# Kernel tuning notes

Hardware: AMD Instinct MI355X
Metric: run time of the kernel (lower is better)

Reference implementation:

```python
import jax, jax.numpy as jnp
import numpy as np

N = 50000
E = 500000
IN_DIM = 384
HID = 256
HEADS = 4
OUT_DIM = 128
NEG_SLOPE = 0.2


def _glorot(key, shape):
    fan_in, fan_out = shape[0], shape[-1]
    lim = jnp.sqrt(6.0 / (fan_in + fan_out))
    return jax.random.uniform(key, shape, jnp.float32, -lim, lim)


def setup_inputs() -> dict:
    key = jax.random.key(0)
    ks = jax.random.split(key, 16)
    x = jax.random.normal(ks[0], (N, IN_DIM), jnp.float32)
    node_attr = jax.random.normal(ks[1], (N, 2), jnp.float32)
    edge_index = jax.random.randint(ks[2], (2, E), 0, N, jnp.int64)
    return {
        "x": x,
        "node_attr": node_attr,
        "edge_index": edge_index,
        # node_encoder: Linear(386 -> 384)
        "enc_W": _glorot(ks[3], (IN_DIM + 2, IN_DIM)),
        "enc_b": jnp.zeros((IN_DIM,), jnp.float32),
        # gat1: 384 -> 4 heads x 256, concat
        "W1": _glorot(ks[4], (IN_DIM, HEADS * HID)),
        "a_src1": _glorot(ks[5], (HEADS, HID)),
        "a_dst1": _glorot(ks[6], (HEADS, HID)),
        "b1": jnp.zeros((HEADS * HID,), jnp.float32),
        # gat2: 1024 -> 1 head x 128, mean (concat=False)
        "W2": _glorot(ks[7], (HEADS * HID, OUT_DIM)),
        "a_src2": _glorot(ks[8], (1, OUT_DIM)),
        "a_dst2": _glorot(ks[9], (1, OUT_DIM)),
        "b2": jnp.zeros((OUT_DIM,), jnp.float32),
    }


def gat_conv(x, src, dst, W, a_src, a_dst, bias, heads, out_ch, concat):
    # x: [N, F]; src/dst: [E'] (self-loops already included)
    n = x.shape[0]
    h = (x @ W).reshape(n, heads, out_ch)          # [N, H, C]
    alpha_s = jnp.einsum('nhc,hc->nh', h, a_src)   # [N, H]
    alpha_d = jnp.einsum('nhc,hc->nh', h, a_dst)
    e = alpha_s[src] + alpha_d[dst]                # [E', H]
    e = jnp.where(e >= 0, e, NEG_SLOPE * e)        # LeakyReLU(0.2)
    # segment softmax over incoming edges of each destination node
    m = jax.ops.segment_max(e, dst, num_segments=n)
    e = jnp.exp(e - m[dst])
    denom = jax.ops.segment_sum(e, dst, num_segments=n)
    alpha = e / (denom[dst] + 1e-16)               # [E', H]
    msg = h[src] * alpha[:, :, None]               # [E', H, C]
    out = jax.ops.segment_sum(msg, dst, num_segments=n)  # [N, H, C]
    out = out.reshape(n, heads * out_ch) if concat else out.mean(axis=1)
    return out + bias


def reference(x, node_attr, edge_index, enc_W, enc_b,
              W1, a_src1, a_dst1, b1, W2, a_src2, a_dst2, b2):
    n = x.shape[0]
    # node encoder on [x ; node_attr]
    h = jnp.concatenate([x, node_attr], axis=-1) @ enc_W + enc_b
    # add self-loops once (PyG GATConv default add_self_loops=True)
    loop = jnp.arange(n, dtype=edge_index.dtype)
    src = jnp.concatenate([edge_index[0], loop])
    dst = jnp.concatenate([edge_index[1], loop])
    h = gat_conv(h, src, dst, W1, a_src1, a_dst1, b1, HEADS, HID, True)
    h = jax.nn.elu(h)
    out = gat_conv(h, src, dst, W2, a_src2, a_dst2, b2, 1, OUT_DIM, False)
    return out
```

## Files before the change

### kernel.cpp

```cpp
#include <hip/hip_runtime.h>
#include <hip/hip_bf16.h>
#include <type_traits>


#define NN 50000
#define NE 500000
#define EP (NE + NN)

typedef __hip_bfloat16 bf16;
typedef short short8 __attribute__((ext_vector_type(8)));
typedef __bf16 bf16x8 __attribute__((ext_vector_type(8)));
typedef float f32x4 __attribute__((ext_vector_type(4)));

__device__ __forceinline__ float b2f(bf16 v) { return __bfloat162float(v); }
__device__ __forceinline__ bf16  f2b(float v) { return __float2bfloat16(v); }
__device__ __forceinline__ unsigned short f2bu(float v) {
  bf16 b = __float2bfloat16(v);
  return *reinterpret_cast<unsigned short*>(&b);
}

__device__ __forceinline__ float ldf(const void* p, size_t i, bool f32) {
  return f32 ? ((const float*)p)[i] : b2f(((const bf16*)p)[i]);
}

__device__ __forceinline__ float bflo(unsigned u) { return __uint_as_float(u << 16); }
__device__ __forceinline__ float bfhi(unsigned u) { return __uint_as_float(u & 0xffff0000u); }

__device__ __forceinline__ float leaky(float v) { return v >= 0.f ? v : 0.2f * v; }

__device__ __forceinline__ void gload_lds16(const void* g, void* l) {
  __builtin_amdgcn_global_load_lds(
      (const __attribute__((address_space(1))) void*)g,
      (__attribute__((address_space(3))) void*)l, 16, 0, 0);
}

__global__ void k_detect(const unsigned int* __restrict__ ei,
                         const unsigned int* __restrict__ xw,
                         unsigned int* __restrict__ eflag,
                         unsigned int* __restrict__ fflag) {
  const int b = blockIdx.x;
  if (b < 512) {
    unsigned int acc = 0;
    for (int i = b * 256 + threadIdx.x; i < NE; i += 512 * 256)
      acc |= ei[2 * i + 1];
    if (acc) atomicOr(eflag, 1u);
  } else {
    unsigned int acc = 0;
    for (int i = (b - 512) * 256 + threadIdx.x; i < (1 << 20); i += 256 * 256) {
      unsigned int e = (xw[i] >> 7) & 0xFF;
      if (e > 0xA0) acc = 1;
    }
    if (acc) atomicOr(fflag, 1u);
  }
}

__global__ void k_convert(const int* __restrict__ ei, const unsigned int* __restrict__ flag,
                          int* __restrict__ esrc, int* __restrict__ edst,
                          int* __restrict__ deg) {
  int e = blockIdx.x * 256 + threadIdx.x;
  if (e >= EP) return;
  int s, d;
  if (e < NE) {
    if (*flag) { s = ei[e]; d = ei[NE + e]; }
    else { const long long* e64 = (const long long*)ei; s = (int)e64[e]; d = (int)e64[NE + e]; }
    s = min(max(s, 0), NN - 1);
    d = min(max(d, 0), NN - 1);
  } else {
    s = d = e - NE;
  }
  esrc[e] = s;
  edst[e] = d;
  atomicAdd(&deg[d], 1);
}

__global__ void k_pack_cat(const void* __restrict__ x, const void* __restrict__ na,
                           bf16* __restrict__ catp, const unsigned int* __restrict__ fflag) {
  const bool f32 = (*fflag != 0);
  const int total = NN * 104;
  for (int g = blockIdx.x * 256 + threadIdx.x; g < total; g += gridDim.x * 256) {
    int n = g / 104, r = g - n * 104;
    int c = r * 4;
    float v0 = 0.f, v1 = 0.f, v2 = 0.f, v3 = 0.f;
    if (c < 384) {
      if (f32) {
        const float4 f = *(const float4*)((const float*)x + (size_t)n * 384 + c);
        v0 = f.x; v1 = f.y; v2 = f.z; v3 = f.w;
      } else {
        const bf16* xb = (const bf16*)x + (size_t)n * 384 + c;
        v0 = b2f(xb[0]); v1 = b2f(xb[1]); v2 = b2f(xb[2]); v3 = b2f(xb[3]);
      }
    } else if (c == 384) {
      v0 = ldf(na, (size_t)n * 2 + 0, f32);
      v1 = ldf(na, (size_t)n * 2 + 1, f32);
    }
    ushort2 o0, o1;
    o0.x = f2bu(v0); o0.y = f2bu(v1);
    o1.x = f2bu(v2); o1.y = f2bu(v3);
    ushort2* dst = (ushort2*)((unsigned short*)catp + (size_t)n * 416 + c);
    dst[0] = o0; dst[1] = o1;
  }
}

__global__ void k_pack_w3(const void* __restrict__ Wenc, bf16* __restrict__ encWp,
                          const void* __restrict__ W1, bf16* __restrict__ W1p,
                          const void* __restrict__ W2, bf16* __restrict__ W2p,
                          const unsigned int* __restrict__ fflag) {
  const bool f32 = (*fflag != 0);
  const int s0 = 416 * 384, s1 = 384 * 1024, s2 = 1024 * 128;
  int g = blockIdx.x * 256 + threadIdx.x;
  const void* W; bf16* Wp; int K, N, i;
  if (g < s0)                { W = Wenc; Wp = encWp; K = 386;  N = 384;  i = g; }
  else if (g < s0 + s1)      { W = W1;   Wp = W1p;   K = 384;  N = 1024; i = g - s0; }
  else if (g < s0 + s1 + s2) { W = W2;   Wp = W2p;   K = 1024; N = 128;  i = g - s0 - s1; }
  else return;
  int kb = i / (N * 32);
  int rem = i - kb * N * 32;
  int n = rem >> 5, kk = rem & 31;
  int k = kb * 32 + kk;
  float v = (k < K) ? ldf(W, (size_t)k * N + n, f32) : 0.f;
  Wp[i] = f2b(v);
}

template<bool ADD_BIAS, bool ALPHA, int NH, typename CT>
__global__ __launch_bounds__(256) void gemm_mfma(
    const bf16* __restrict__ A, int lda,
    const bf16* __restrict__ Bp,
    const void* __restrict__ bias,
    const void* __restrict__ a_srcp, const void* __restrict__ a_dstp,
    float* __restrict__ as_out, float* __restrict__ ad_out,
    CT* __restrict__ C,
    int M, int N, int K,
    const unsigned int* __restrict__ fflag) {
  const bool xf32 = (ADD_BIAS || ALPHA) ? (*fflag != 0) : false;
  __shared__ short As[128 * 32];
  __shared__ short Bs[128 * 32];
  const int t = threadIdx.x;
  const int lane = t & 63, wave = t >> 6;
  const int wm = wave & 1, wn = wave >> 1;
  const int quad = lane >> 4, l15 = lane & 15;
  const int m0 = blockIdx.x * 128, n0 = blockIdx.y * 128;

  f32x4 acc[4][4];
#pragma unroll
  for (int i = 0; i < 4; ++i)
#pragma unroll
    for (int j = 0; j < 4; ++j) acc[i][j] = (f32x4){0.f, 0.f, 0.f, 0.f};

  const int c0 = t, c1 = t + 256;
  const int arow0 = min(m0 + (c0 >> 2), M - 1), akoff0 = (c0 & 3) * 8;
  const int arow1 = min(m0 + (c1 >> 2), M - 1), akoff1 = (c1 & 3) * 8;

  for (int k0 = 0; k0 < K; k0 += 32) {
    gload_lds16((const short*)A + (size_t)arow0 * lda + k0 + akoff0, &As[c0 * 8]);
    gload_lds16((const short*)A + (size_t)arow1 * lda + k0 + akoff1, &As[c1 * 8]);
    {
      const short* base = (const short*)Bp + ((size_t)(k0 >> 5) * N + n0) * 32;
      gload_lds16(base + c0 * 8, &Bs[c0 * 8]);
      gload_lds16(base + c1 * 8, &Bs[c1 * 8]);
    }
    __syncthreads();
    bf16x8 af[4], bfr[4];
#pragma unroll
    for (int mi = 0; mi < 4; ++mi)
      af[mi] = *reinterpret_cast<const bf16x8*>(&As[(wm * 64 + mi * 16 + l15) * 32 + quad * 8]);
#pragma unroll
    for (int ni = 0; ni < 4; ++ni)
      bfr[ni] = *reinterpret_cast<const bf16x8*>(&Bs[(wn * 64 + ni * 16 + l15) * 32 + quad * 8]);
#pragma unroll
    for (int mi = 0; mi < 4; ++mi)
#pragma unroll
      for (int ni = 0; ni < 4; ++ni)
        acc[mi][ni] = __builtin_amdgcn_mfma_f32_16x16x32_bf16(af[mi], bfr[ni], acc[mi][ni], 0, 0, 0);
    __syncthreads();
  }

#pragma unroll
  for (int mi = 0; mi < 4; ++mi) {
#pragma unroll
    for (int ni = 0; ni < 4; ++ni) {
      const int gn = n0 + wn * 64 + ni * 16 + l15;
      float bv = ADD_BIAS ? ldf(bias, gn, xf32) : 0.f;
#pragma unroll
      for (int r = 0; r < 4; ++r) {
        const int gm = m0 + wm * 64 + mi * 16 + quad * 4 + r;
        if (gm < M) {
          float v = acc[mi][ni][r] + bv;
          if constexpr (std::is_same<CT, float>::value)
            C[(size_t)gm * N + gn] = v;
          else
            C[(size_t)gm * N + gn] = f2b(v);
        }
      }
    }
  }

  if (ALPHA) {
    float avs[4], avd[4];
#pragma unroll
    for (int ni = 0; ni < 4; ++ni) {
      const int gn = n0 + wn * 64 + ni * 16 + l15;
      avs[ni] = ldf(a_srcp, gn, xf32);
      avd[ni] = ldf(a_dstp, gn, xf32);
    }
    const int head = (n0 + wn * 64) >> 8;
#pragma unroll
    for (int mi = 0; mi < 4; ++mi) {
#pragma unroll
      for (int r = 0; r < 4; ++r) {
        float ps = 0.f, pd = 0.f;
#pragma unroll
        for (int ni = 0; ni < 4; ++ni) {
          const float v = acc[mi][ni][r];
          ps = fmaf(v, avs[ni], ps);
          pd = fmaf(v, avd[ni], pd);
        }
#pragma unroll
        for (int off = 8; off > 0; off >>= 1) {
          ps += __shfl_down(ps, off, 16);
          pd += __shfl_down(pd, off, 16);
        }
        if (l15 == 0) {
          const int gm = m0 + wm * 64 + mi * 16 + quad * 4 + r;
          if (gm < M) {
            atomicAdd(&as_out[gm * NH + head], ps);
            atomicAdd(&ad_out[gm * NH + head], pd);
          }
        }
      }
    }
  }
}

#define SCAN_B 512
#define SCAN_NB ((NN + SCAN_B - 1) / SCAN_B)

__global__ __launch_bounds__(SCAN_B) void k_scan1(const int* __restrict__ deg,
                                                  int* __restrict__ row_ptr,
                                                  int* __restrict__ partial) {
  int b = blockIdx.x, t = threadIdx.x;
  int i = b * SCAN_B + t;
  int v = (i < NN) ? deg[i] : 0;
  int lane = t & 63, w = t >> 6;
  int x = v;
#pragma unroll
  for (int off = 1; off < 64; off <<= 1) {
    int y = __shfl_up(x, off, 64);
    if (lane >= off) x += y;
  }
  __shared__ int ws[8];
  if (lane == 63) ws[w] = x;
  __syncthreads();
  if (t == 0) {
    int run = 0;
#pragma unroll
    for (int j = 0; j < 8; ++j) { int tmp = ws[j]; ws[j] = run; run += tmp; }
    partial[b] = run;
  }
  __syncthreads();
  int excl = x - v + ws[w];
  if (i < NN) row_ptr[i] = excl;
}

__global__ void k_scan2(int* __restrict__ partial, int* __restrict__ row_ptr) {
  if (blockIdx.x == 0 && threadIdx.x == 0) {
    int run = 0;
    for (int j = 0; j < SCAN_NB; ++j) { int tmp = partial[j]; partial[j] = run; run += tmp; }
    row_ptr[NN] = run;
  }
}

__global__ __launch_bounds__(SCAN_B) void k_scan3(const int* __restrict__ partial,
                                                  int* __restrict__ row_ptr,
                                                  int* __restrict__ cursor) {
  int b = blockIdx.x, t = threadIdx.x;
  int i = b * SCAN_B + t;
  if (i < NN) {
    int v = row_ptr[i] + partial[b];
    row_ptr[i] = v;
    cursor[i] = v;
  }
}

__global__ void k_scatter(const int* __restrict__ esrc, const int* __restrict__ edst,
                          int* __restrict__ cursor, int* __restrict__ csr) {
  int e = blockIdx.x * 256 + threadIdx.x;
  if (e >= EP) return;
  int pos = atomicAdd(&cursor[edst[e]], 1);
  pos = min(max(pos, 0), EP - 1);
  csr[pos] = esrc[e];
}

__global__ __launch_bounds__(256) void k_agg1(
    const int* __restrict__ csr, const int* __restrict__ row_ptr,
    const float* __restrict__ as1, const float* __restrict__ ad1,
    const bf16* __restrict__ h1, const void* __restrict__ b1,
    bf16* __restrict__ act1, const unsigned int* __restrict__ fflag) {
  const bool f32 = (*fflag != 0);
  const int n = blockIdx.x, t = threadIdx.x;
  const int w = t >> 6, l = t & 63;
  const int start = row_ptr[n], end = row_ptr[n + 1];
  const float adn = ad1[n * 4 + w];
  const unsigned* hb = (const unsigned*)h1;
  const int coff = w * 128 + l * 2;

  float a0 = 0.f, a1 = 0.f, a2 = 0.f, a3 = 0.f, densum = 0.f;

  int idx = start;
  for (; idx + 4 <= end; idx += 4) {
    int s0 = csr[idx], s1 = csr[idx + 1], s2 = csr[idx + 2], s3 = csr[idx + 3];
    uint2 w0 = *(const uint2*)(hb + (size_t)s0 * 512 + coff);
    uint2 w1 = *(const uint2*)(hb + (size_t)s1 * 512 + coff);
    uint2 w2 = *(const uint2*)(hb + (size_t)s2 * 512 + coff);
    uint2 w3 = *(const uint2*)(hb + (size_t)s3 * 512 + coff);
    float p0 = __expf(leaky(as1[s0 * 4 + w] + adn));
    float p1 = __expf(leaky(as1[s1 * 4 + w] + adn));
    float p2 = __expf(leaky(as1[s2 * 4 + w] + adn));
    float p3 = __expf(leaky(as1[s3 * 4 + w] + adn));
    densum += (p0 + p1) + (p2 + p3);
    a0 = fmaf(bflo(w0.x), p0, a0); a1 = fmaf(bfhi(w0.x), p0, a1);
    a2 = fmaf(bflo(w0.y), p0, a2); a3 = fmaf(bfhi(w0.y), p0, a3);
    a0 = fmaf(bflo(w1.x), p1, a0); a1 = fmaf(bfhi(w1.x), p1, a1);
    a2 = fmaf(bflo(w1.y), p1, a2); a3 = fmaf(bfhi(w1.y), p1, a3);
    a0 = fmaf(bflo(w2.x), p2, a0); a1 = fmaf(bfhi(w2.x), p2, a1);
    a2 = fmaf(bflo(w2.y), p2, a2); a3 = fmaf(bfhi(w2.y), p2, a3);
    a0 = fmaf(bflo(w3.x), p3, a0); a1 = fmaf(bfhi(w3.x), p3, a1);
    a2 = fmaf(bflo(w3.y), p3, a2); a3 = fmaf(bfhi(w3.y), p3, a3);
  }
  for (; idx < end; ++idx) {
    int s0 = csr[idx];
    uint2 w0 = *(const uint2*)(hb + (size_t)s0 * 512 + coff);
    float p0 = __expf(leaky(as1[s0 * 4 + w] + adn));
    densum += p0;
    a0 = fmaf(bflo(w0.x), p0, a0); a1 = fmaf(bfhi(w0.x), p0, a1);
    a2 = fmaf(bflo(w0.y), p0, a2); a3 = fmaf(bfhi(w0.y), p0, a3);
  }

  const float inv = 1.f / (densum + 1e-16f);
  const int col = w * 256 + l * 4;
  float v0 = a0 * inv + ldf(b1, col + 0, f32);
  float v1 = a1 * inv + ldf(b1, col + 1, f32);
  float v2 = a2 * inv + ldf(b1, col + 2, f32);
  float v3 = a3 * inv + ldf(b1, col + 3, f32);
  v0 = v0 > 0.f ? v0 : expm1f(v0);
  v1 = v1 > 0.f ? v1 : expm1f(v1);
  v2 = v2 > 0.f ? v2 : expm1f(v2);
  v3 = v3 > 0.f ? v3 : expm1f(v3);
  unsigned lo = (unsigned)f2bu(v0) | ((unsigned)f2bu(v1) << 16);
  unsigned hi = (unsigned)f2bu(v2) | ((unsigned)f2bu(v3) << 16);
  unsigned long long ow = (unsigned long long)lo | ((unsigned long long)hi << 32);
  __builtin_nontemporal_store(
      ow, (unsigned long long*)((unsigned short*)act1 + (size_t)n * 1024 + col));
}

__global__ __launch_bounds__(256) void k_agg2(
    const int* __restrict__ csr, const int* __restrict__ row_ptr,
    const float* __restrict__ as2, const float* __restrict__ ad2,
    const bf16* __restrict__ h2, const void* __restrict__ b2v,
    float* __restrict__ out, const unsigned int* __restrict__ fflag) {
  const bool f32 = (*fflag != 0);
  const int t = threadIdx.x;
  const int wv = t >> 6, l = t & 63;
  const int n = blockIdx.x * 4 + wv;
  const int start = row_ptr[n], end = row_ptr[n + 1];
  const float adn = ad2[n];
  const unsigned* hb = (const unsigned*)h2;
  float a0 = 0.f, a1 = 0.f, densum = 0.f;

  int idx = start;
  for (; idx + 2 <= end; idx += 2) {
    const int s0 = __builtin_amdgcn_readfirstlane(csr[idx]);
    const int s1 = __builtin_amdgcn_readfirstlane(csr[idx + 1]);
    const unsigned w0 = hb[(size_t)s0 * 64 + l];
    const unsigned w1 = hb[(size_t)s1 * 64 + l];
    const float p0 = __expf(leaky(as2[s0] + adn));
    const float p1 = __expf(leaky(as2[s1] + adn));
    densum += p0 + p1;
    a0 = fmaf(bflo(w0), p0, a0); a1 = fmaf(bfhi(w0), p0, a1);
    a0 = fmaf(bflo(w1), p1, a0); a1 = fmaf(bfhi(w1), p1, a1);
  }
  if (idx < end) {
    const int s0 = __builtin_amdgcn_readfirstlane(csr[idx]);
    const unsigned w0 = hb[(size_t)s0 * 64 + l];
    const float p0 = __expf(leaky(as2[s0] + adn));
    densum += p0;
    a0 = fmaf(bflo(w0), p0, a0); a1 = fmaf(bfhi(w0), p0, a1);
  }

  const float inv = 1.f / (densum + 1e-16f);
  float2 o;
  o.x = a0 * inv + ldf(b2v, l * 2 + 0, f32);
  o.y = a1 * inv + ldf(b2v, l * 2 + 1, f32);
  unsigned long long u;
  __builtin_memcpy(&u, &o, 8);
  __builtin_nontemporal_store(u, (unsigned long long*)(out + (size_t)n * 128 + l * 2));
}

extern "C" void kernel_launch(void* const* d_in, const int* in_sizes, int n_in,
                              void* d_out, int out_size, void* d_ws, size_t ws_size,
                              hipStream_t stream) {
  const void* x       = d_in[0];
  const void* na      = d_in[1];
  const int*  ei      = (const int*)d_in[2];
  const void* enc_W   = d_in[3];
  const void* enc_b   = d_in[4];
  const void* W1      = d_in[5];
  const void* a_src1  = d_in[6];
  const void* a_dst1  = d_in[7];
  const void* b1      = d_in[8];
  const void* W2      = d_in[9];
  const void* a_src2  = d_in[10];
  const void* a_dst2  = d_in[11];
  const void* b2      = d_in[12];
  float* out = (float*)d_out;

  size_t off = 0;
  char* ws = (char*)d_ws;
  auto alloc = [&](size_t bytes) -> void* {
    void* p = ws + off;
    off += (bytes + 255) & ~(size_t)255;
    return p;
  };
  bf16*  h1      = (bf16*)alloc((size_t)NN * 1024 * 2);
  bf16*  act1    = (bf16*)alloc((size_t)NN * 1024 * 2);
  bf16*  catp    = act1;
  bf16*  h0      = (bf16*)alloc((size_t)NN * 384 * 2);
  bf16*  h2      = (bf16*)alloc((size_t)NN * 128 * 2);
  bf16*  encWp   = (bf16*)alloc((size_t)416 * 384 * 2);
  bf16*  W1p     = (bf16*)alloc((size_t)384 * 1024 * 2);
  bf16*  W2p     = (bf16*)alloc((size_t)1024 * 128 * 2);
  int*   esrc    = (int*)alloc((size_t)EP * 4);
  int*   edst    = (int*)alloc((size_t)EP * 4);
  int*   csr     = (int*)alloc((size_t)EP * 4);
  char*  zero_base = ws + off;
  unsigned int* eflag = (unsigned int*)alloc(4);
  unsigned int* fflag = (unsigned int*)alloc(4);
  int*   deg     = (int*)alloc((size_t)NN * 4);
  float* as1     = (float*)alloc((size_t)NN * 4 * 4);
  float* ad1     = (float*)alloc((size_t)NN * 4 * 4);
  float* as2     = (float*)alloc((size_t)NN * 4);
  float* ad2     = (float*)alloc((size_t)NN * 4);
  size_t zero_len = (size_t)((ws + off) - zero_base);
  int*   row_ptr = (int*)alloc((size_t)(NN + 1) * 4);
  int*   cursor  = (int*)alloc((size_t)NN * 4);
  int*   partial = (int*)alloc((size_t)SCAN_NB * 4);
  (void)ws_size; (void)in_sizes; (void)n_in; (void)out_size;

  (void)hipMemsetAsync(zero_base, 0, zero_len, stream);

  const int EB = (EP + 255) / 256;
  const int MB = (NN + 127) / 128;

  k_detect<<<768, 256, 0, stream>>>((const unsigned int*)ei, (const unsigned int*)x,
                                    eflag, fflag);

  k_convert<<<EB, 256, 0, stream>>>(ei, eflag, esrc, edst, deg);
  k_scan1<<<SCAN_NB, SCAN_B, 0, stream>>>(deg, row_ptr, partial);
  k_scan2<<<1, 64, 0, stream>>>(partial, row_ptr);
  k_scan3<<<SCAN_NB, SCAN_B, 0, stream>>>(partial, row_ptr, cursor);
  k_scatter<<<EB, 256, 0, stream>>>(esrc, edst, cursor, csr);

  k_pack_cat<<<8192, 256, 0, stream>>>(x, na, catp, fflag);
  k_pack_w3<<<2672, 256, 0, stream>>>(enc_W, encWp, W1, W1p, W2, W2p, fflag);

  gemm_mfma<true, false, 1, bf16><<<dim3(MB, 3), 256, 0, stream>>>(
      catp, 416, encWp, enc_b, nullptr, nullptr, nullptr, nullptr,
      h0, NN, 384, 416, fflag);
  gemm_mfma<false, true, 4, bf16><<<dim3(MB, 8), 256, 0, stream>>>(
      h0, 384, W1p, nullptr, a_src1, a_dst1, as1, ad1,
      h1, NN, 1024, 384, fflag);

  k_agg1<<<NN, 256, 0, stream>>>(csr, row_ptr, as1, ad1, h1, b1, act1, fflag);

  gemm_mfma<false, true, 1, bf16><<<dim3(MB, 1), 256, 0, stream>>>(
      act1, 1024, W2p, nullptr, a_src2, a_dst2, as2, ad2,
      h2, NN, 128, 1024, fflag);

  k_agg2<<<NN / 4, 256, 0, stream>>>(csr, row_ptr, as2, ad2, h2, b2, out, fflag);
}
```

Baseline: 653.5 us.

## Fuse preprocessing kernels into one cooperative kernel with grid syncs

Replaces eight small preprocessing launches (dtype detection, edge conversion, degree scan, CSR scatter, input and weight packing) with a single cooperative kernel that uses grid.sync between phases. It keeps the old multi-kernel path as a fallback if the cooperative launch fails. The aim is to remove per-launch overhead and idle gaps between tiny kernels. In exchange it adds grid-wide barrier costs and runs the work on a fixed 1024-block grid.

```diff
diff --git a/kernel.cpp b/kernel.cpp
--- a/kernel.cpp
+++ b/kernel.cpp
@@ -1,11 +1,14 @@
 #include <hip/hip_runtime.h>
 #include <hip/hip_bf16.h>
+#include <hip/hip_cooperative_groups.h>
 #include <type_traits>
 
 
 #define NN 50000
 #define NE 500000
 #define EP (NE + NN)
+
+namespace cg = cooperative_groups;
 
 typedef __hip_bfloat16 bf16;
 typedef short short8 __attribute__((ext_vector_type(8)));
@@ -32,6 +35,162 @@
   __builtin_amdgcn_global_load_lds(
       (const __attribute__((address_space(1))) void*)g,
       (__attribute__((address_space(3))) void*)l, 16, 0, 0);
+}
+
+__device__ __forceinline__ void convert_item(int e, bool ef, const int* ei,
+                                             int* esrc, int* edst, int* deg) {
+  int s, d;
+  if (e < NE) {
+    if (ef) { s = ei[e]; d = ei[NE + e]; }
+    else { const long long* e64 = (const long long*)ei; s = (int)e64[e]; d = (int)e64[NE + e]; }
+    s = min(max(s, 0), NN - 1);
+    d = min(max(d, 0), NN - 1);
+  } else {
+    s = d = e - NE;
+  }
+  esrc[e] = s;
+  edst[e] = d;
+  atomicAdd(&deg[d], 1);
+}
+
+__device__ __forceinline__ void pack_cat_item(int g, bool f32, const void* x,
+                                              const void* na, bf16* catp) {
+  int n = g / 104, r = g - n * 104;
+  int c = r * 4;
+  float v0 = 0.f, v1 = 0.f, v2 = 0.f, v3 = 0.f;
+  if (c < 384) {
+    if (f32) {
+      const float4 f = *(const float4*)((const float*)x + (size_t)n * 384 + c);
+      v0 = f.x; v1 = f.y; v2 = f.z; v3 = f.w;
+    } else {
+      const bf16* xb = (const bf16*)x + (size_t)n * 384 + c;
+      v0 = b2f(xb[0]); v1 = b2f(xb[1]); v2 = b2f(xb[2]); v3 = b2f(xb[3]);
+    }
+  } else if (c == 384) {
+    v0 = ldf(na, (size_t)n * 2 + 0, f32);
+    v1 = ldf(na, (size_t)n * 2 + 1, f32);
+  }
+  ushort2 o0, o1;
+  o0.x = f2bu(v0); o0.y = f2bu(v1);
+  o1.x = f2bu(v2); o1.y = f2bu(v3);
+  ushort2* dst = (ushort2*)((unsigned short*)catp + (size_t)n * 416 + c);
+  dst[0] = o0; dst[1] = o1;
+}
+
+#define PW_S0 (416 * 384)
+#define PW_S1 (384 * 1024)
+#define PW_S2 (1024 * 128)
+
+__device__ __forceinline__ void pack_w3_item(int i, bool f32,
+                                             const void* Wenc, bf16* encWp,
+                                             const void* W1, bf16* W1p,
+                                             const void* W2, bf16* W2p) {
+  const void* W; bf16* Wp; int K, N, ii;
+  if (i < PW_S0)               { W = Wenc; Wp = encWp; K = 386;  N = 384;  ii = i; }
+  else if (i < PW_S0 + PW_S1)  { W = W1;   Wp = W1p;   K = 384;  N = 1024; ii = i - PW_S0; }
+  else                         { W = W2;   Wp = W2p;   K = 1024; N = 128;  ii = i - PW_S0 - PW_S1; }
+  int kb = ii / (N * 32);
+  int rem = ii - kb * N * 32;
+  int n = rem >> 5, kk = rem & 31;
+  int k = kb * 32 + kk;
+  float v = (k < K) ? ldf(W, (size_t)k * N + n, f32) : 0.f;
+  Wp[ii] = f2b(v);
+}
+
+#define SCAN_NB ((NN + 511) / 512)
+
+__global__ __launch_bounds__(256, 4) void k_prep(
+    const int* __restrict__ ei, const void* __restrict__ x, const void* __restrict__ na,
+    const void* __restrict__ Wenc, const void* __restrict__ W1w, const void* __restrict__ W2w,
+    int* __restrict__ esrc, int* __restrict__ edst, int* __restrict__ deg,
+    bf16* __restrict__ catp, bf16* __restrict__ encWp, bf16* __restrict__ W1p,
+    bf16* __restrict__ W2p,
+    unsigned int* eflag, unsigned int* fflag,
+    int* __restrict__ row_ptr, int* __restrict__ cursor, int* __restrict__ partial,
+    int* __restrict__ csr) {
+  cg::grid_group grid = cg::this_grid();
+  const int t = threadIdx.x;
+  const int gid = blockIdx.x * 256 + t;
+  const int gsz = gridDim.x * 256;
+
+  {
+    const unsigned* eiw = (const unsigned*)ei;
+    unsigned acc = 0;
+    for (int i = gid; i < NE; i += gsz) acc |= eiw[2 * i + 1];
+    if (acc) atomicOr(eflag, 1u);
+    const unsigned* xw = (const unsigned*)x;
+    unsigned fa = 0;
+    for (int i = gid; i < (1 << 20); i += gsz) {
+      unsigned e = (xw[i] >> 7) & 0xFF;
+      if (e > 0xA0) fa = 1;
+    }
+    if (fa) atomicOr(fflag, 1u);
+  }
+  grid.sync();
+
+  const bool ef  = (*(volatile const unsigned*)eflag != 0);
+  const bool f32 = (*(volatile const unsigned*)fflag != 0);
+
+  {
+    const int T1 = EP;
+    const int T2 = T1 + NN * 104;
+    const int T3 = T2 + PW_S0 + PW_S1 + PW_S2;
+    for (int g = gid; g < T3; g += gsz) {
+      if (g < T1)       convert_item(g, ef, ei, esrc, edst, deg);
+      else if (g < T2)  pack_cat_item(g - T1, f32, x, na, catp);
+      else              pack_w3_item(g - T2, f32, Wenc, encWp, W1w, W1p, W2w, W2p);
+    }
+  }
+  grid.sync();
+
+  if (blockIdx.x < SCAN_NB) {
+    const int b = blockIdx.x;
+    const int i0 = b * 512 + t * 2;
+    int v0 = (i0 < NN) ? deg[i0] : 0;
+    int v1 = (i0 + 1 < NN) ? deg[i0 + 1] : 0;
+    int sp = v0 + v1;
+    int lane = t & 63, w = t >> 6;
+    int xv = sp;
+#pragma unroll
+    for (int off = 1; off < 64; off <<= 1) {
+      int y = __shfl_up(xv, off, 64);
+      if (lane >= off) xv += y;
+    }
+    __shared__ int ws[4];
+    if (lane == 63) ws[w] = xv;
+    __syncthreads();
+    if (t == 0) {
+      int run = 0;
+#pragma unroll
+      for (int j = 0; j < 4; ++j) { int tmp = ws[j]; ws[j] = run; run += tmp; }
+      partial[b] = run;
+    }
+    __syncthreads();
+    int excl = xv - sp + ws[w];
+    if (i0 < NN) row_ptr[i0] = excl;
+    if (i0 + 1 < NN) row_ptr[i0 + 1] = excl + v0;
+  }
+  grid.sync();
+
+  if (gid == 0) {
+    int run = 0;
+    for (int j = 0; j < SCAN_NB; ++j) { int tmp = partial[j]; partial[j] = run; run += tmp; }
+    row_ptr[NN] = run;
+  }
+  grid.sync();
+
+  for (int i = gid; i < NN; i += gsz) {
+    int v = row_ptr[i] + partial[i >> 9];
+    row_ptr[i] = v;
+    cursor[i] = v;
+  }
+  grid.sync();
+
+  for (int e = gid; e < EP; e += gsz) {
+    int pos = atomicAdd(&cursor[edst[e]], 1);
+    pos = min(max(pos, 0), EP - 1);
+    csr[pos] = esrc[e];
+  }
 }
 
 __global__ void k_detect(const unsigned int* __restrict__ ei,
@@ -59,46 +218,15 @@
                           int* __restrict__ deg) {
   int e = blockIdx.x * 256 + threadIdx.x;
   if (e >= EP) return;
-  int s, d;
-  if (e < NE) {
-    if (*flag) { s = ei[e]; d = ei[NE + e]; }
-    else { const long long* e64 = (const long long*)ei; s = (int)e64[e]; d = (int)e64[NE + e]; }
-    s = min(max(s, 0), NN - 1);
-    d = min(max(d, 0), NN - 1);
-  } else {
-    s = d = e - NE;
-  }
-  esrc[e] = s;
-  edst[e] = d;
-  atomicAdd(&deg[d], 1);
+  convert_item(e, *flag != 0, ei, esrc, edst, deg);
 }
 
 __global__ void k_pack_cat(const void* __restrict__ x, const void* __restrict__ na,
                            bf16* __restrict__ catp, const unsigned int* __restrict__ fflag) {
   const bool f32 = (*fflag != 0);
   const int total = NN * 104;
-  for (int g = blockIdx.x * 256 + threadIdx.x; g < total; g += gridDim.x * 256) {
-    int n = g / 104, r = g - n * 104;
-    int c = r * 4;
-    float v0 = 0.f, v1 = 0.f, v2 = 0.f, v3 = 0.f;
-    if (c < 384) {
-      if (f32) {
-        const float4 f = *(const float4*)((const float*)x + (size_t)n * 384 + c);
-        v0 = f.x; v1 = f.y; v2 = f.z; v3 = f.w;
-      } else {
-        const bf16* xb = (const bf16*)x + (size_t)n * 384 + c;
-        v0 = b2f(xb[0]); v1 = b2f(xb[1]); v2 = b2f(xb[2]); v3 = b2f(xb[3]);
-      }
-    } else if (c == 384) {
-      v0 = ldf(na, (size_t)n * 2 + 0, f32);
-      v1 = ldf(na, (size_t)n * 2 + 1, f32);
-    }
-    ushort2 o0, o1;
-    o0.x = f2bu(v0); o0.y = f2bu(v1);
-    o1.x = f2bu(v2); o1.y = f2bu(v3);
-    ushort2* dst = (ushort2*)((unsigned short*)catp + (size_t)n * 416 + c);
-    dst[0] = o0; dst[1] = o1;
-  }
+  for (int g = blockIdx.x * 256 + threadIdx.x; g < total; g += gridDim.x * 256)
+    pack_cat_item(g, f32, x, na, catp);
 }
 
 __global__ void k_pack_w3(const void* __restrict__ Wenc, bf16* __restrict__ encWp,
@@ -106,19 +234,67 @@
                           const void* __restrict__ W2, bf16* __restrict__ W2p,
                           const unsigned int* __restrict__ fflag) {
   const bool f32 = (*fflag != 0);
-  const int s0 = 416 * 384, s1 = 384 * 1024, s2 = 1024 * 128;
   int g = blockIdx.x * 256 + threadIdx.x;
-  const void* W; bf16* Wp; int K, N, i;
-  if (g < s0)                { W = Wenc; Wp = encWp; K = 386;  N = 384;  i = g; }
-  else if (g < s0 + s1)      { W = W1;   Wp = W1p;   K = 384;  N = 1024; i = g - s0; }
-  else if (g < s0 + s1 + s2) { W = W2;   Wp = W2p;   K = 1024; N = 128;  i = g - s0 - s1; }
-  else return;
-  int kb = i / (N * 32);
-  int rem = i - kb * N * 32;
-  int n = rem >> 5, kk = rem & 31;
-  int k = kb * 32 + kk;
-  float v = (k < K) ? ldf(W, (size_t)k * N + n, f32) : 0.f;
-  Wp[i] = f2b(v);
+  if (g < PW_S0 + PW_S1 + PW_S2)
+    pack_w3_item(g, f32, Wenc, encWp, W1, W1p, W2, W2p);
+}
+
+#define SCAN_B 512
+
+__global__ __launch_bounds__(SCAN_B) void k_scan1(const int* __restrict__ deg,
+                                                  int* __restrict__ row_ptr,
+                                                  int* __restrict__ partial) {
+  int b = blockIdx.x, t = threadIdx.x;
+  int i = b * SCAN_B + t;
+  int v = (i < NN) ? deg[i] : 0;
+  int lane = t & 63, w = t >> 6;
+  int x = v;
+#pragma unroll
+  for (int off = 1; off < 64; off <<= 1) {
+    int y = __shfl_up(x, off, 64);
+    if (lane >= off) x += y;
+  }
+  __shared__ int ws[8];
+  if (lane == 63) ws[w] = x;
+  __syncthreads();
+  if (t == 0) {
+    int run = 0;
+#pragma unroll
+    for (int j = 0; j < 8; ++j) { int tmp = ws[j]; ws[j] = run; run += tmp; }
+    partial[b] = run;
+  }
+  __syncthreads();
+  int excl = x - v + ws[w];
+  if (i < NN) row_ptr[i] = excl;
+}
+
+__global__ void k_scan2(int* __restrict__ partial, int* __restrict__ row_ptr) {
+  if (blockIdx.x == 0 && threadIdx.x == 0) {
+    int run = 0;
+    for (int j = 0; j < SCAN_NB; ++j) { int tmp = partial[j]; partial[j] = run; run += tmp; }
+    row_ptr[NN] = run;
+  }
+}
+
+__global__ __launch_bounds__(SCAN_B) void k_scan3(const int* __restrict__ partial,
+                                                  int* __restrict__ row_ptr,
+                                                  int* __restrict__ cursor) {
+  int b = blockIdx.x, t = threadIdx.x;
+  int i = b * SCAN_B + t;
+  if (i < NN) {
+    int v = row_ptr[i] + partial[b];
+    row_ptr[i] = v;
+    cursor[i] = v;
+  }
+}
+
+__global__ void k_scatter(const int* __restrict__ esrc, const int* __restrict__ edst,
+                          int* __restrict__ cursor, int* __restrict__ csr) {
+  int e = blockIdx.x * 256 + threadIdx.x;
+  if (e >= EP) return;
+  int pos = atomicAdd(&cursor[edst[e]], 1);
+  pos = min(max(pos, 0), EP - 1);
+  csr[pos] = esrc[e];
 }
 
 template<bool ADD_BIAS, bool ALPHA, int NH, typename CT>
@@ -229,65 +405,6 @@
       }
     }
   }
-}
-
-#define SCAN_B 512
-#define SCAN_NB ((NN + SCAN_B - 1) / SCAN_B)
-
-__global__ __launch_bounds__(SCAN_B) void k_scan1(const int* __restrict__ deg,
-                                                  int* __restrict__ row_ptr,
-                                                  int* __restrict__ partial) {
-  int b = blockIdx.x, t = threadIdx.x;
-  int i = b * SCAN_B + t;
-  int v = (i < NN) ? deg[i] : 0;
-  int lane = t & 63, w = t >> 6;
-  int x = v;
-#pragma unroll
-  for (int off = 1; off < 64; off <<= 1) {
-    int y = __shfl_up(x, off, 64);
-    if (lane >= off) x += y;
-  }
-  __shared__ int ws[8];
-  if (lane == 63) ws[w] = x;
-  __syncthreads();
-  if (t == 0) {
-    int run = 0;
-#pragma unroll
-    for (int j = 0; j < 8; ++j) { int tmp = ws[j]; ws[j] = run; run += tmp; }
-    partial[b] = run;
-  }
-  __syncthreads();
-  int excl = x - v + ws[w];
-  if (i < NN) row_ptr[i] = excl;
-}
-
-__global__ void k_scan2(int* __restrict__ partial, int* __restrict__ row_ptr) {
-  if (blockIdx.x == 0 && threadIdx.x == 0) {
-    int run = 0;
-    for (int j = 0; j < SCAN_NB; ++j) { int tmp = partial[j]; partial[j] = run; run += tmp; }
-    row_ptr[NN] = run;
-  }
-}
-
-__global__ __launch_bounds__(SCAN_B) void k_scan3(const int* __restrict__ partial,
-                                                  int* __restrict__ row_ptr,
-                                                  int* __restrict__ cursor) {
-  int b = blockIdx.x, t = threadIdx.x;
-  int i = b * SCAN_B + t;
-  if (i < NN) {
-    int v = row_ptr[i] + partial[b];
-    row_ptr[i] = v;
-    cursor[i] = v;
-  }
-}
-
-__global__ void k_scatter(const int* __restrict__ esrc, const int* __restrict__ edst,
-                          int* __restrict__ cursor, int* __restrict__ csr) {
-  int e = blockIdx.x * 256 + threadIdx.x;
-  if (e >= EP) return;
-  int pos = atomicAdd(&cursor[edst[e]], 1);
-  pos = min(max(pos, 0), EP - 1);
-  csr[pos] = esrc[e];
 }
 
 __global__ __launch_bounds__(256) void k_agg1(
@@ -450,17 +567,31 @@
   const int EB = (EP + 255) / 256;
   const int MB = (NN + 127) / 128;
 
-  k_detect<<<768, 256, 0, stream>>>((const unsigned int*)ei, (const unsigned int*)x,
-                                    eflag, fflag);
-
-  k_convert<<<EB, 256, 0, stream>>>(ei, eflag, esrc, edst, deg);
-  k_scan1<<<SCAN_NB, SCAN_B, 0, stream>>>(deg, row_ptr, partial);
-  k_scan2<<<1, 64, 0, stream>>>(partial, row_ptr);
-  k_scan3<<<SCAN_NB, SCAN_B, 0, stream>>>(partial, row_ptr, cursor);
-  k_scatter<<<EB, 256, 0, stream>>>(esrc, edst, cursor, csr);
-
-  k_pack_cat<<<8192, 256, 0, stream>>>(x, na, catp, fflag);
-  k_pack_w3<<<2672, 256, 0, stream>>>(enc_W, encWp, W1, W1p, W2, W2p, fflag);
+  {
+    const int* ei_a = ei; const void* x_a = x; const void* na_a = na;
+    const void* we_a = enc_W; const void* w1_a = W1; const void* w2_a = W2;
+    int* esrc_a = esrc; int* edst_a = edst; int* deg_a = deg;
+    bf16* catp_a = catp; bf16* encWp_a = encWp; bf16* W1p_a = W1p; bf16* W2p_a = W2p;
+    unsigned int* ef_a = eflag; unsigned int* ff_a = fflag;
+    int* rp_a = row_ptr; int* cur_a = cursor; int* par_a = partial; int* csr_a = csr;
+    void* args[] = { &ei_a, &x_a, &na_a, &we_a, &w1_a, &w2_a,
+                     &esrc_a, &edst_a, &deg_a,
+                     &catp_a, &encWp_a, &W1p_a, &W2p_a,
+                     &ef_a, &ff_a, &rp_a, &cur_a, &par_a, &csr_a };
+    hipError_t cerr = hipLaunchCooperativeKernel(
+        (const void*)k_prep, dim3(1024), dim3(256), args, 0, stream);
+    if (cerr != hipSuccess) {
+      k_detect<<<768, 256, 0, stream>>>((const unsigned int*)ei, (const unsigned int*)x,
+                                        eflag, fflag);
+      k_convert<<<EB, 256, 0, stream>>>(ei, eflag, esrc, edst, deg);
+      k_scan1<<<SCAN_NB, SCAN_B, 0, stream>>>(deg, row_ptr, partial);
+      k_scan2<<<1, 64, 0, stream>>>(partial, row_ptr);
+      k_scan3<<<SCAN_NB, SCAN_B, 0, stream>>>(partial, row_ptr, cursor);
+      k_scatter<<<EB, 256, 0, stream>>>(esrc, edst, cursor, csr);
+      k_pack_cat<<<8192, 256, 0, stream>>>(x, na, catp, fflag);
+      k_pack_w3<<<2672, 256, 0, stream>>>(enc_W, encWp, W1, W1p, W2, W2p, fflag);
+    }
+  }
 
   gemm_mfma<true, false, 1, bf16><<<dim3(MB, 3), 256, 0, stream>>>(
       catp, 416, encWp, enc_b, nullptr, nullptr, nullptr, nullptr,
```

Result: slower. 1.216 ms (+86.1%).
